# Optimization experiments

Hardware: AMD Instinct MI355X
Metric: run time of the kernel (lower is better)

Reference implementation:

```python
import jax, jax.numpy as jnp
import numpy as np

N_NODES = 100000
N_EDGES = 1600000
IN_C = 256
H1 = 128
H2 = 64
OUT_C = 64


def setup_inputs() -> dict:
    key = jax.random.key(0)
    ks = jax.random.split(key, 8)
    x = jax.random.normal(ks[0], (N_NODES, IN_C), dtype=jnp.float32)
    edge_src = jax.random.randint(ks[1], (N_EDGES,), 0, N_NODES, dtype=jnp.int32)
    edge_dst = jax.random.randint(ks[2], (N_EDGES,), 0, N_NODES, dtype=jnp.int32)
    edge_weight = jax.random.uniform(ks[3], (N_EDGES,), dtype=jnp.float32)
    W1 = jax.random.normal(ks[4], (IN_C, H1), dtype=jnp.float32) / np.sqrt(IN_C)
    b1 = jnp.zeros((H1,), dtype=jnp.float32)
    W2 = jax.random.normal(ks[5], (H1, H2), dtype=jnp.float32) / np.sqrt(H1)
    b2 = jnp.zeros((H2,), dtype=jnp.float32)
    W3 = jax.random.normal(ks[6], (H2, OUT_C), dtype=jnp.float32) / np.sqrt(H2)
    b3 = jnp.zeros((OUT_C,), dtype=jnp.float32)
    return dict(x=x, edge_src=edge_src, edge_dst=edge_dst, edge_weight=edge_weight,
                W1=W1, b1=b1, W2=W2, b2=b2, W3=W3, b3=b3)


def _gcn_layer(h, W, b, src, dst, ew):
    # GraphConvolution: out = adj @ (h @ W) + b, adj given as weighted edge list
    support = h @ W                      # [N, d_out] dense GEMM
    msg = support[src] * ew[:, None]     # [E, d_out] gather (irregular access)
    agg = jax.ops.segment_sum(msg, dst, num_segments=N_NODES)  # SpMM scatter-add
    return agg + b


def reference(x, edge_src, edge_dst, edge_weight, W1, b1, W2, b2, W3, b3):
    # Eval-mode forward: dropout is identity (training=False)
    h = jax.nn.relu(_gcn_layer(x, W1, b1, edge_src, edge_dst, edge_weight))
    h = jax.nn.relu(_gcn_layer(h, W2, b2, edge_src, edge_dst, edge_weight))
    out = _gcn_layer(h, W3, b3, edge_src, edge_dst, edge_weight)
    return out
```

## Files before the change

### kernel.cpp

```cpp
#include <hip/hip_runtime.h>
#include <hip/hip_bf16.h>


#define EPB 8192

__device__ __forceinline__ unsigned short f2bf(float f) {
    unsigned int u = __float_as_uint(f);
    unsigned int r = (u + 0x7fffu + ((u >> 16) & 1u)) >> 16;
    return (unsigned short)r;
}

using frag_ab = __attribute__((ext_vector_type(8))) short;
using frag_cd = __attribute__((ext_vector_type(4))) float;

template <int BN, int K, bool ABF16>
__global__ __launch_bounds__(256) void mfma_gemm_kernel(
    const void* __restrict__ Av, const unsigned short* __restrict__ WT,
    unsigned short* __restrict__ C, int M)
{
    constexpr int BM = 64, BK = 64;
    constexpr int NT = K / BK;
    constexpr int LDB = BK + 8;
    constexpr int BLD = BN / 32;
    __shared__ unsigned short Bs[BN * LDB];

    const int tid = threadIdx.x;
    const int wave = tid >> 6;
    const int lane = tid & 63;
    const int quad = lane >> 4;
    const int l16 = lane & 15;
    const int m0 = blockIdx.x * BM;

    const int r0 = m0 + wave * 16 + l16;
    const bool rv = r0 < M;

    frag_cd acc[BN / 16];
#pragma unroll
    for (int f = 0; f < BN / 16; ++f) acc[f] = (frag_cd){0.f, 0.f, 0.f, 0.f};

    const float* Af = (const float*)Av;
    const unsigned short* Ah = (const unsigned short*)Av;

    uint4 breg[BLD];
    float4 arf[2][2];
    frag_ab arh[2];

    auto loadB = [&](int k0) {
#pragma unroll
        for (int i = 0; i < BLD; ++i) {
            const int linear = (i * 256 + tid) * 8;
            const int n = linear >> 6;
            const int c = linear & 63;
            breg[i] = *(const uint4*)&WT[(size_t)n * K + k0 + c];
        }
    };
    auto writeB = [&]() {
#pragma unroll
        for (int i = 0; i < BLD; ++i) {
            const int linear = (i * 256 + tid) * 8;
            const int n = linear >> 6;
            const int c = linear & 63;
            *(uint4*)&Bs[n * LDB + c] = breg[i];
        }
    };
    auto loadA = [&](int k0) {
        if constexpr (!ABF16) {
            const float* base = &Af[(size_t)r0 * K + k0 + quad * 8];
#pragma unroll
            for (int ks = 0; ks < 2; ++ks) {
                float4 lo = make_float4(0.f, 0.f, 0.f, 0.f);
                float4 hi = make_float4(0.f, 0.f, 0.f, 0.f);
                if (rv) {
                    lo = *(const float4*)(base + ks * 32);
                    hi = *(const float4*)(base + ks * 32 + 4);
                }
                arf[ks][0] = lo;
                arf[ks][1] = hi;
            }
        } else {
            const unsigned short* base = &Ah[(size_t)r0 * K + k0 + quad * 8];
#pragma unroll
            for (int ks = 0; ks < 2; ++ks) {
                frag_ab f = (frag_ab){0, 0, 0, 0, 0, 0, 0, 0};
                if (rv) f = *(const frag_ab*)(base + ks * 32);
                arh[ks] = f;
            }
        }
    };

    loadB(0);
    loadA(0);

    for (int t = 0; t < NT; ++t) {
        writeB();
        __syncthreads();

        frag_ab af[2];
#pragma unroll
        for (int ks = 0; ks < 2; ++ks) {
            if constexpr (!ABF16) {
                const float4 lo = arf[ks][0];
                const float4 hi = arf[ks][1];
                frag_ab f;
                f[0] = (short)f2bf(lo.x); f[1] = (short)f2bf(lo.y);
                f[2] = (short)f2bf(lo.z); f[3] = (short)f2bf(lo.w);
                f[4] = (short)f2bf(hi.x); f[5] = (short)f2bf(hi.y);
                f[6] = (short)f2bf(hi.z); f[7] = (short)f2bf(hi.w);
                af[ks] = f;
            } else {
                af[ks] = arh[ks];
            }
        }
        if (t + 1 < NT) {
            loadB((t + 1) * BK);
            loadA((t + 1) * BK);
        }

#pragma unroll
        for (int ks = 0; ks < 2; ++ks) {
            const int kk = ks * 32 + quad * 8;
#pragma unroll
            for (int f = 0; f < BN / 16; ++f) {
                const frag_ab b = *(const frag_ab*)&Bs[(f * 16 + l16) * LDB + kk];
                acc[f] = __builtin_amdgcn_mfma_f32_16x16x32_bf16(af[ks], b, acc[f], 0, 0, 0);
            }
        }
        __syncthreads();
    }

#pragma unroll
    for (int f = 0; f < BN / 16; ++f)
#pragma unroll
        for (int r = 0; r < 4; ++r) {
            const int row = m0 + wave * 16 + quad * 4 + r;
            if (row < M) C[(size_t)row * BN + f * 16 + l16] = f2bf(acc[f][r]);
        }
}

__global__ __launch_bounds__(256) void wt_kernel(
    const float* __restrict__ W1, const float* __restrict__ W2, const float* __restrict__ W3,
    unsigned short* __restrict__ WT1, unsigned short* __restrict__ WT2, unsigned short* __restrict__ WT3)
{
    const int i = blockIdx.x * 256 + threadIdx.x;
    const float* W; unsigned short* WT; int K, N, j;
    if (i < 32768)      { W = W1; WT = WT1; K = 256; N = 128; j = i; }
    else if (i < 40960) { W = W2; WT = WT2; K = 128; N = 64;  j = i - 32768; }
    else if (i < 45056) { W = W3; WT = WT3; K = 64;  N = 64;  j = i - 40960; }
    else return;
    const int n = j / K, k = j % K;
    WT[j] = f2bf(W[k * N + n]);
}

__global__ __launch_bounds__(256) void count_kernel(
    const int* __restrict__ dst, int* __restrict__ cmat, int E, int nblk, int nbuck)
{
    __shared__ int hist[1600];
    for (int i = threadIdx.x; i < nbuck; i += 256) hist[i] = 0;
    __syncthreads();
    const int base = blockIdx.x * EPB;
    const int end = min(base + EPB, E);
    for (int e = base + threadIdx.x; e < end; e += 256)
        atomicAdd(&hist[dst[e] >> 6], 1);
    __syncthreads();
    for (int i = threadIdx.x; i < nbuck; i += 256)
        cmat[(size_t)i * nblk + blockIdx.x] = hist[i];
}

__global__ __launch_bounds__(256) void scanA_kernel(
    int* __restrict__ data, int* __restrict__ psum, int L)
{
    __shared__ int tmp[256];
    const int b0 = blockIdx.x * 1024 + threadIdx.x * 4;
    int v[4] = {0, 0, 0, 0};
    if (b0 + 3 < L) { const int4 t = *(const int4*)&data[b0]; v[0]=t.x; v[1]=t.y; v[2]=t.z; v[3]=t.w; }
    else { for (int i = 0; i < 4; ++i) if (b0 + i < L) v[i] = data[b0 + i]; }
    const int s = v[0] + v[1] + v[2] + v[3];
    tmp[threadIdx.x] = s;
    __syncthreads();
#pragma unroll
    for (int d = 1; d < 256; d <<= 1) {
        const int t = (threadIdx.x >= d) ? tmp[threadIdx.x - d] : 0;
        __syncthreads();
        tmp[threadIdx.x] += t;
        __syncthreads();
    }
    int run = tmp[threadIdx.x] - s;
    int o[4];
#pragma unroll
    for (int i = 0; i < 4; ++i) { o[i] = run; run += v[i]; }
    if (b0 + 3 < L) { *(int4*)&data[b0] = make_int4(o[0], o[1], o[2], o[3]); }
    else { for (int i = 0; i < 4; ++i) if (b0 + i < L) data[b0 + i] = o[i]; }
    if (threadIdx.x == 255) psum[blockIdx.x] = tmp[255];
}

__global__ __launch_bounds__(1024) void scanB_kernel(int* __restrict__ psum, int nb)
{
    __shared__ int tmp[1024];
    const int v = ((int)threadIdx.x < nb) ? psum[threadIdx.x] : 0;
    tmp[threadIdx.x] = v;
    __syncthreads();
#pragma unroll
    for (int d = 1; d < 1024; d <<= 1) {
        const int t = ((int)threadIdx.x >= d) ? tmp[threadIdx.x - d] : 0;
        __syncthreads();
        tmp[threadIdx.x] += t;
        __syncthreads();
    }
    if ((int)threadIdx.x < nb) psum[threadIdx.x] = tmp[threadIdx.x] - v;
}

__global__ __launch_bounds__(256) void scanC_kernel(
    int* __restrict__ data, const int* __restrict__ psum, int L)
{
    const int i = blockIdx.x * 256 + threadIdx.x;
    if (i < L) data[i] += psum[i >> 10];
}

__global__ __launch_bounds__(256) void place_kernel(
    const int* __restrict__ src, const int* __restrict__ dst, const float* __restrict__ ew,
    const int* __restrict__ cmat, uint2* __restrict__ ebuck, int E, int nblk, int nbuck)
{
    __shared__ int cursor[1600];
    const int k = blockIdx.x;
    for (int i = threadIdx.x; i < nbuck; i += 256)
        cursor[i] = cmat[(size_t)i * nblk + k];
    __syncthreads();
    const int base = k * EPB;
    const int end = min(base + EPB, E);
    for (int e = base + threadIdx.x; e < end; e += 256) {
        const int d = dst[e];
        const int b = d >> 6;
        const int pos = atomicAdd(&cursor[b], 1);
        ebuck[pos] = make_uint2(((unsigned)src[e] << 6) | (unsigned)(d & 63),
                                __float_as_uint(ew[e]));
    }
}

__global__ __launch_bounds__(256) void sort2_kernel(
    const uint2* __restrict__ ebuck, const int* __restrict__ cmat,
    int* __restrict__ offs, uint2* __restrict__ ecsr,
    int N, int nblk, int nbuck, int E)
{
    __shared__ int cnt[64];
    __shared__ int cur[64];
    const int b = blockIdx.x;
    const int node0 = b << 6;
    const int nn = min(64, N - node0);
    const int j0 = cmat[(size_t)b * nblk];
    const int j1 = (b + 1 < nbuck) ? cmat[(size_t)(b + 1) * nblk] : E;

    if (threadIdx.x < 64) cnt[threadIdx.x] = 0;
    __syncthreads();
    for (int j = j0 + (int)threadIdx.x; j < j1; j += 256)
        atomicAdd(&cnt[ebuck[j].x & 63u], 1);
    __syncthreads();

    if (threadIdx.x < 64) {
        const int myv = cnt[threadIdx.x];
        int v = myv;
#pragma unroll
        for (int d = 1; d < 64; d <<= 1) {
            const int t = __shfl_up(v, d, 64);
            if ((int)threadIdx.x >= d) v += t;
        }
        const int base = j0 + v - myv;
        cur[threadIdx.x] = base;
        if ((int)threadIdx.x < nn) offs[node0 + threadIdx.x] = base;
        if (threadIdx.x == 0 && b == nbuck - 1) offs[N] = E;
    }
    __syncthreads();

    for (int j = j0 + (int)threadIdx.x; j < j1; j += 256) {
        const uint2 ed = ebuck[j];
        const int pos = atomicAdd(&cur[ed.x & 63u], 1);
        ecsr[pos] = make_uint2(ed.x >> 6, ed.y);
    }
}

template <int D, int LOGT, bool RELU, typename OUT_T>
__global__ __launch_bounds__(256) void gather_agg_kernel(
    const unsigned short* __restrict__ S, const int* __restrict__ offs,
    const uint2* __restrict__ ecsr,
    const float* __restrict__ bias, OUT_T* __restrict__ out, int N)
{
    constexpr int TPN = 1 << LOGT;
    const int gid = blockIdx.x * 256 + threadIdx.x;
    const int node = gid >> LOGT;
    if (node >= N) return;
    const int lane = gid & (TPN - 1);
    const int c8 = lane << 3;

    const int j0 = offs[node];
    const int j1 = offs[node + 1];

    float acc[8];
#pragma unroll
    for (int c = 0; c < 8; ++c) acc[c] = 0.f;

    const int nchunk = (j1 - j0 + TPN - 1) >> LOGT;
    int jb = j0;
    for (int ch = 0; ch < nchunk; ++ch, jb += TPN) {
        const int j = jb + lane;
        int myc = 0;
        float myw = 0.f;
        if (j < j1) {
            const uint2 p = ecsr[j];
            myc = (int)p.x;
            myw = __uint_as_float(p.y);
        }
#pragma unroll
        for (int t = 0; t < TPN; ++t) {
            const int s = __shfl(myc, t, TPN);
            const float w = __shfl(myw, t, TPN);
            const uint4 v = *(const uint4*)&S[(size_t)s * D + c8];
#pragma unroll
            for (int q = 0; q < 4; ++q) {
                const unsigned int u = (&v.x)[q];
                acc[q * 2 + 0] += w * __uint_as_float(u << 16);
                acc[q * 2 + 1] += w * __uint_as_float(u & 0xffff0000u);
            }
        }
    }

#pragma unroll
    for (int c = 0; c < 8; ++c) {
        float v = acc[c] + bias[c8 + c];
        if (RELU) v = fmaxf(v, 0.f);
        acc[c] = v;
    }
    if constexpr (sizeof(OUT_T) == 2) {
        uint4 u;
        u.x = ((unsigned)f2bf(acc[1]) << 16) | (unsigned)f2bf(acc[0]);
        u.y = ((unsigned)f2bf(acc[3]) << 16) | (unsigned)f2bf(acc[2]);
        u.z = ((unsigned)f2bf(acc[5]) << 16) | (unsigned)f2bf(acc[4]);
        u.w = ((unsigned)f2bf(acc[7]) << 16) | (unsigned)f2bf(acc[6]);
        *(uint4*)&((unsigned short*)out)[(size_t)node * D + c8] = u;
    } else {
        float* op = (float*)out + (size_t)node * D + c8;
        *(float4*)op = make_float4(acc[0], acc[1], acc[2], acc[3]);
        *((float4*)op + 1) = make_float4(acc[4], acc[5], acc[6], acc[7]);
    }
}

extern "C" void kernel_launch(void* const* d_in, const int* in_sizes, int n_in,
                              void* d_out, int out_size, void* d_ws, size_t ws_size,
                              hipStream_t stream)
{
    const float* x    = (const float*)d_in[0];
    const int*   esrc = (const int*)  d_in[1];
    const int*   edst = (const int*)  d_in[2];
    const float* ew   = (const float*)d_in[3];
    const float* W1   = (const float*)d_in[4];
    const float* b1   = (const float*)d_in[5];
    const float* W2   = (const float*)d_in[6];
    const float* b2   = (const float*)d_in[7];
    const float* W3   = (const float*)d_in[8];
    const float* b3   = (const float*)d_in[9];

    const int N = in_sizes[0] / 256;
    const int E = in_sizes[1];

    const int nbuck = (N + 63) >> 6;
    const int nblk = (E + EPB - 1) / EPB;
    const int L = nbuck * nblk;

    unsigned short* Sb = (unsigned short*)d_ws;
    unsigned short* Hb = Sb + (size_t)N * 128;
    unsigned short* WT1 = Hb + (size_t)N * 128;
    unsigned short* WT2 = WT1 + 256 * 128;
    unsigned short* WT3 = WT2 + 128 * 64;
    uint2* ebuck = (uint2*)(WT3 + 64 * 64);
    uint2* ecsr  = ebuck + E;
    int* offs   = (int*)(ecsr + E);
    int* cmat   = offs + N + 4;
    int* psum   = cmat + ((L + 3) & ~3);
    float* out  = (float*)d_out;

    const dim3 blk(256);
    const int mblocks = (N + 63) / 64;

    wt_kernel<<<(45056 + 255) / 256, blk, 0, stream>>>(W1, W2, W3, WT1, WT2, WT3);
    count_kernel<<<nblk, blk, 0, stream>>>(edst, cmat, E, nblk, nbuck);
    scanA_kernel<<<(L + 1023) / 1024, blk, 0, stream>>>(cmat, psum, L);
    scanB_kernel<<<1, 1024, 0, stream>>>(psum, (L + 1023) / 1024);
    scanC_kernel<<<(L + 255) / 256, blk, 0, stream>>>(cmat, psum, L);
    place_kernel<<<nblk, blk, 0, stream>>>(esrc, edst, ew, cmat, ebuck, E, nblk, nbuck);
    sort2_kernel<<<nbuck, blk, 0, stream>>>(ebuck, cmat, offs, ecsr, N, nblk, nbuck, E);

    mfma_gemm_kernel<128, 256, false><<<mblocks, blk, 0, stream>>>(x, WT1, Sb, N);
    gather_agg_kernel<128, 4, true, unsigned short><<<((N * 16) + 255) / 256, blk, 0, stream>>>(
        Sb, offs, ecsr, b1, Hb, N);

    mfma_gemm_kernel<64, 128, true><<<mblocks, blk, 0, stream>>>(Hb, WT2, Sb, N);
    gather_agg_kernel<64, 3, true, unsigned short><<<((N * 8) + 255) / 256, blk, 0, stream>>>(
        Sb, offs, ecsr, b2, Hb, N);

    mfma_gemm_kernel<64, 64, true><<<mblocks, blk, 0, stream>>>(Hb, WT3, Sb, N);
    gather_agg_kernel<64, 3, false, float><<<((N * 8) + 255) / 256, blk, 0, stream>>>(
        Sb, offs, ecsr, b3, out, N);
}
```

Measured before the change: 493.6 us.

## Keep full weight matrix resident in LDS and loop waves over row tiles

Replaces the K-tiled, double-buffered GEMM with a kernel that loads the entire transposed weight matrix into shared memory once per block. Each wave then independently walks 16-row tiles without block-wide barriers. The first layer uses a persistent grid of 512 blocks with 8 waves. This removes the per-K-step syncs and the repeated weight staging, at the cost of larger LDS use (about 67KB for layer 1), which may limit occupancy, and less latency hiding of A loads.

Measured after the change: 462.8 us. 6.2% less time.

```diff
diff --git a/kernel.cpp b/kernel.cpp
--- a/kernel.cpp
+++ b/kernel.cpp
@@ -13,15 +13,15 @@
 using frag_ab = __attribute__((ext_vector_type(8))) short;
 using frag_cd = __attribute__((ext_vector_type(4))) float;
 
-template <int BN, int K, bool ABF16>
-__global__ __launch_bounds__(256) void mfma_gemm_kernel(
+template <int BN, int K, bool ABF16, int WAVES>
+__global__ __launch_bounds__(WAVES * 64) void wgemm_kernel(
     const void* __restrict__ Av, const unsigned short* __restrict__ WT,
     unsigned short* __restrict__ C, int M)
 {
-    constexpr int BM = 64, BK = 64;
-    constexpr int NT = K / BK;
-    constexpr int LDB = BK + 8;
-    constexpr int BLD = BN / 32;
+    constexpr int LDB = K + 8;
+    constexpr int NKS = K / 32;
+    constexpr int KB = (NKS >= 4) ? 4 : NKS;
+    constexpr int NB = NKS / KB;
     __shared__ unsigned short Bs[BN * LDB];
 
     const int tid = threadIdx.x;
@@ -29,112 +29,86 @@
     const int lane = tid & 63;
     const int quad = lane >> 4;
     const int l16 = lane & 15;
-    const int m0 = blockIdx.x * BM;
-
-    const int r0 = m0 + wave * 16 + l16;
-    const bool rv = r0 < M;
-
-    frag_cd acc[BN / 16];
-#pragma unroll
-    for (int f = 0; f < BN / 16; ++f) acc[f] = (frag_cd){0.f, 0.f, 0.f, 0.f};
+
+    constexpr int NTHR = WAVES * 64;
+    constexpr int TOT = BN * K / 8;
+    for (int i = tid; i < TOT; i += NTHR) {
+        const int n = (i << 3) / K;
+        const int c = (i << 3) & (K - 1);
+        *(uint4*)&Bs[n * LDB + c] = *(const uint4*)&WT[(size_t)n * K + c];
+    }
+    __syncthreads();
 
     const float* Af = (const float*)Av;
     const unsigned short* Ah = (const unsigned short*)Av;
 
-    uint4 breg[BLD];
-    float4 arf[2][2];
-    frag_ab arh[2];
-
-    auto loadB = [&](int k0) {
-#pragma unroll
-        for (int i = 0; i < BLD; ++i) {
-            const int linear = (i * 256 + tid) * 8;
-            const int n = linear >> 6;
-            const int c = linear & 63;
-            breg[i] = *(const uint4*)&WT[(size_t)n * K + k0 + c];
-        }
-    };
-    auto writeB = [&]() {
-#pragma unroll
-        for (int i = 0; i < BLD; ++i) {
-            const int linear = (i * 256 + tid) * 8;
-            const int n = linear >> 6;
-            const int c = linear & 63;
-            *(uint4*)&Bs[n * LDB + c] = breg[i];
-        }
-    };
-    auto loadA = [&](int k0) {
-        if constexpr (!ABF16) {
-            const float* base = &Af[(size_t)r0 * K + k0 + quad * 8];
-#pragma unroll
-            for (int ks = 0; ks < 2; ++ks) {
-                float4 lo = make_float4(0.f, 0.f, 0.f, 0.f);
-                float4 hi = make_float4(0.f, 0.f, 0.f, 0.f);
-                if (rv) {
-                    lo = *(const float4*)(base + ks * 32);
-                    hi = *(const float4*)(base + ks * 32 + 4);
+    const int tiles = (M + 15) >> 4;
+    for (int tile = blockIdx.x * WAVES + wave; tile < tiles; tile += gridDim.x * WAVES) {
+        const int r0 = tile * 16 + l16;
+        const bool rv = r0 < M;
+
+        frag_cd acc[BN / 16];
+#pragma unroll
+        for (int f = 0; f < BN / 16; ++f) acc[f] = (frag_cd){0.f, 0.f, 0.f, 0.f};
+
+#pragma unroll
+        for (int b = 0; b < NB; ++b) {
+            frag_ab af[KB];
+            if constexpr (!ABF16) {
+                const float* base = &Af[(size_t)r0 * K + quad * 8];
+                float4 arf[KB][2];
+#pragma unroll
+                for (int k = 0; k < KB; ++k) {
+                    const int ks = b * KB + k;
+                    float4 lo = make_float4(0.f, 0.f, 0.f, 0.f);
+                    float4 hi = make_float4(0.f, 0.f, 0.f, 0.f);
+                    if (rv) {
+                        lo = *(const float4*)(base + ks * 32);
+                        hi = *(const float4*)(base + ks * 32 + 4);
+                    }
+                    arf[k][0] = lo;
+                    arf[k][1] = hi;
                 }
-                arf[ks][0] = lo;
-                arf[ks][1] = hi;
+#pragma unroll
+                for (int k = 0; k < KB; ++k) {
+                    const float4 lo = arf[k][0];
+                    const float4 hi = arf[k][1];
+                    frag_ab f8;
+                    f8[0] = (short)f2bf(lo.x); f8[1] = (short)f2bf(lo.y);
+                    f8[2] = (short)f2bf(lo.z); f8[3] = (short)f2bf(lo.w);
+                    f8[4] = (short)f2bf(hi.x); f8[5] = (short)f2bf(hi.y);
+                    f8[6] = (short)f2bf(hi.z); f8[7] = (short)f2bf(hi.w);
+                    af[k] = f8;
+                }
+            } else {
+                const unsigned short* base = &Ah[(size_t)r0 * K + quad * 8];
+#pragma unroll
+                for (int k = 0; k < KB; ++k) {
+                    const int ks = b * KB + k;
+                    frag_ab f8 = (frag_ab){0, 0, 0, 0, 0, 0, 0, 0};
+                    if (rv) f8 = *(const frag_ab*)(base + ks * 32);
+                    af[k] = f8;
+                }
             }
-        } else {
-            const unsigned short* base = &Ah[(size_t)r0 * K + k0 + quad * 8];
-#pragma unroll
-            for (int ks = 0; ks < 2; ++ks) {
-                frag_ab f = (frag_ab){0, 0, 0, 0, 0, 0, 0, 0};
-                if (rv) f = *(const frag_ab*)(base + ks * 32);
-                arh[ks] = f;
+#pragma unroll
+            for (int k = 0; k < KB; ++k) {
+                const int kk = (b * KB + k) * 32 + quad * 8;
+#pragma unroll
+                for (int f = 0; f < BN / 16; ++f) {
+                    const frag_ab bf = *(const frag_ab*)&Bs[(f * 16 + l16) * LDB + kk];
+                    acc[f] = __builtin_amdgcn_mfma_f32_16x16x32_bf16(af[k], bf, acc[f], 0, 0, 0);
+                }
             }
         }
-    };
-
-    loadB(0);
-    loadA(0);
-
-    for (int t = 0; t < NT; ++t) {
-        writeB();
-        __syncthreads();
-
-        frag_ab af[2];
-#pragma unroll
-        for (int ks = 0; ks < 2; ++ks) {
-            if constexpr (!ABF16) {
-                const float4 lo = arf[ks][0];
-                const float4 hi = arf[ks][1];
-                frag_ab f;
-                f[0] = (short)f2bf(lo.x); f[1] = (short)f2bf(lo.y);
-                f[2] = (short)f2bf(lo.z); f[3] = (short)f2bf(lo.w);
-                f[4] = (short)f2bf(hi.x); f[5] = (short)f2bf(hi.y);
-                f[6] = (short)f2bf(hi.z); f[7] = (short)f2bf(hi.w);
-                af[ks] = f;
-            } else {
-                af[ks] = arh[ks];
+
+#pragma unroll
+        for (int f = 0; f < BN / 16; ++f)
+#pragma unroll
+            for (int r = 0; r < 4; ++r) {
+                const int row = tile * 16 + quad * 4 + r;
+                if (row < M) C[(size_t)row * BN + f * 16 + l16] = f2bf(acc[f][r]);
             }
-        }
-        if (t + 1 < NT) {
-            loadB((t + 1) * BK);
-            loadA((t + 1) * BK);
-        }
-
-#pragma unroll
-        for (int ks = 0; ks < 2; ++ks) {
-            const int kk = ks * 32 + quad * 8;
-#pragma unroll
-            for (int f = 0; f < BN / 16; ++f) {
-                const frag_ab b = *(const frag_ab*)&Bs[(f * 16 + l16) * LDB + kk];
-                acc[f] = __builtin_amdgcn_mfma_f32_16x16x32_bf16(af[ks], b, acc[f], 0, 0, 0);
-            }
-        }
-        __syncthreads();
-    }
-
-#pragma unroll
-    for (int f = 0; f < BN / 16; ++f)
-#pragma unroll
-        for (int r = 0; r < 4; ++r) {
-            const int row = m0 + wave * 16 + quad * 4 + r;
-            if (row < M) C[(size_t)row * BN + f * 16 + l16] = f2bf(acc[f][r]);
-        }
+    }
 }
 
 __global__ __launch_bounds__(256) void wt_kernel(
@@ -377,7 +351,7 @@
     float* out  = (float*)d_out;
 
     const dim3 blk(256);
-    const int mblocks = (N + 63) / 64;
+    const int tiles = (N + 15) >> 4;
 
     wt_kernel<<<(45056 + 255) / 256, blk, 0, stream>>>(W1, W2, W3, WT1, WT2, WT3);
     count_kernel<<<nblk, blk, 0, stream>>>(edst, cmat, E, nblk, nbuck);
@@ -387,15 +361,15 @@
     place_kernel<<<nblk, blk, 0, stream>>>(esrc, edst, ew, cmat, ebuck, E, nblk, nbuck);
     sort2_kernel<<<nbuck, blk, 0, stream>>>(ebuck, cmat, offs, ecsr, N, nblk, nbuck, E);
 
-    mfma_gemm_kernel<128, 256, false><<<mblocks, blk, 0, stream>>>(x, WT1, Sb, N);
+    wgemm_kernel<128, 256, false, 8><<<512, dim3(512), 0, stream>>>(x, WT1, Sb, N);
     gather_agg_kernel<128, 4, true, unsigned short><<<((N * 16) + 255) / 256, blk, 0, stream>>>(
         Sb, offs, ecsr, b1, Hb, N);
 
-    mfma_gemm_kernel<64, 128, true><<<mblocks, blk, 0, stream>>>(Hb, WT2, Sb, N);
+    wgemm_kernel<64, 128, true, 4><<<(tiles + 3) / 4, blk, 0, stream>>>(Hb, WT2, Sb, N);
     gather_agg_kernel<64, 3, true, unsigned short><<<((N * 8) + 255) / 256, blk, 0, stream>>>(
         Sb, offs, ecsr, b2, Hb, N);
 
-    mfma_gemm_kernel<64, 64, true><<<mblocks, blk, 0, stream>>>(Hb, WT3, Sb, N);
+    wgemm_kernel<64, 64, true, 4><<<(tiles + 3) / 4, blk, 0, stream>>>(Hb, WT3, Sb, N);
     gather_agg_kernel<64, 3, false, float><<<((N * 8) + 255) / 256, blk, 0, stream>>>(
         Sb, offs, ecsr, b3, out, N);
 }
```
